# Optimization experiments

Measured on AMD Instinct MI355X. Metric: run time of the kernel, lower is better.

## Reference

```python
import jax, jax.numpy as jnp
import numpy as np
from functools import partial

N_NODES = 50000
N_EDGES = 800000
N_ENT = 100000
N_REL = 500
N_POS = 7            # sub_graph_hop_num + 2
DIM = 128            # node_emb_dim == rel_emb_dim == hidden_dim
HEADS = 8
HEAD_DIM = DIM // HEADS
HOPS = 3             # gnn_hop_num
ALPHA = 0.15
FFN_DIM = 4 * DIM
BATCH = 512
SLOPE = 0.2          # leaky relu negative slope


def _ln(x, g, b):
    mu = jnp.mean(x, axis=-1, keepdims=True)
    var = jnp.var(x, axis=-1, keepdims=True)
    return (x - mu) * jax.lax.rsqrt(var + 1e-5) * g + b


def _gdt_layer(h, src, dst, Wh, ah, at, g1, b1, w1, c1, w2, c2, g2, b2,
               rel_score=None):
    """Graph diffusion-transformer layer: edge-softmax attention + PPR hops."""
    N = h.shape[0]
    f = (h @ Wh).reshape(N, HEADS, HEAD_DIM)          # [N,H,Dh]
    s_src = jnp.sum(f * ah, axis=-1)                  # [N,H]
    s_dst = jnp.sum(f * at, axis=-1)                  # [N,H]
    e = s_src[src] + s_dst[dst]                       # [E,H]
    if rel_score is not None:
        e = e + rel_score
    e = jnp.where(e >= 0, e, SLOPE * e)               # leaky relu
    m = jax.ops.segment_max(e, dst, num_segments=N)   # [N,H]
    m = jnp.where(jnp.isfinite(m), m, 0.0)
    ex = jnp.exp(e - m[dst])
    den = jax.ops.segment_sum(ex, dst, num_segments=N)
    att = ex / (den[dst] + 1e-16)                     # [E,H] edge softmax

    feat0 = f
    def hop(feat, _):
        msg = feat[src] * att[:, :, None]             # [E,H,Dh]
        agg = jax.ops.segment_sum(msg, dst, num_segments=N)
        return ALPHA * feat0 + (1.0 - ALPHA) * agg, None
    feat, _ = jax.lax.scan(hop, feat0, None, length=HOPS)

    o = feat.reshape(N, DIM)
    o = _ln(o + h, g1, b1)                            # residual + LN
    ff = jax.nn.relu(o @ w1 + c1) @ w2 + c2           # FFN
    return _ln(o + ff, g2, b2)


def setup_inputs() -> dict:
    key = jax.random.key(0)
    ks = jax.random.split(key, 32)
    s = 0.05
    inp = {
        'ent_ids': jax.random.randint(ks[0], (N_NODES,), 0, N_ENT),
        'rel_ids': jax.random.randint(ks[1], (N_EDGES,), 0, N_REL),
        'arw_pos': jax.random.randint(ks[2], (N_NODES,), 0, N_POS),
        'src': jax.random.randint(ks[3], (N_EDGES,), 0, N_NODES),
        'dst': jax.random.randint(ks[4], (N_EDGES,), 0, N_NODES),
        'batch_node_ids': jax.random.randint(ks[5], (BATCH,), 0, N_NODES),
        'ent_tab': jax.random.normal(ks[6], (N_ENT, DIM)) * s,
        'rel_tab': jax.random.normal(ks[7], (N_REL, DIM)) * s,
        'pos_tab': jax.random.normal(ks[8], (N_POS, DIM)) * s,
        # layer 0 (RGDT: uses relation features)
        'l0_Wh': jax.random.normal(ks[9], (DIM, DIM)) * s,
        'l0_Wr': jax.random.normal(ks[10], (DIM, DIM)) * s,
        'l0_ah': jax.random.normal(ks[11], (HEADS, HEAD_DIM)) * s,
        'l0_at': jax.random.normal(ks[12], (HEADS, HEAD_DIM)) * s,
        'l0_ar': jax.random.normal(ks[13], (HEADS, HEAD_DIM)) * s,
        'l0_g1': jnp.ones((DIM,)), 'l0_b1': jnp.zeros((DIM,)),
        'l0_w1': jax.random.normal(ks[14], (DIM, FFN_DIM)) * s,
        'l0_c1': jnp.zeros((FFN_DIM,)),
        'l0_w2': jax.random.normal(ks[15], (FFN_DIM, DIM)) * s,
        'l0_c2': jnp.zeros((DIM,)),
        'l0_g2': jnp.ones((DIM,)), 'l0_b2': jnp.zeros((DIM,)),
        # layer 1 (GDT: no relation features)
        'l1_Wh': jax.random.normal(ks[16], (DIM, DIM)) * s,
        'l1_ah': jax.random.normal(ks[17], (HEADS, HEAD_DIM)) * s,
        'l1_at': jax.random.normal(ks[18], (HEADS, HEAD_DIM)) * s,
        'l1_g1': jnp.ones((DIM,)), 'l1_b1': jnp.zeros((DIM,)),
        'l1_w1': jax.random.normal(ks[19], (DIM, FFN_DIM)) * s,
        'l1_c1': jnp.zeros((FFN_DIM,)),
        'l1_w2': jax.random.normal(ks[20], (FFN_DIM, DIM)) * s,
        'l1_c2': jnp.zeros((DIM,)),
        'l1_g2': jnp.ones((DIM,)), 'l1_b2': jnp.zeros((DIM,)),
    }
    return inp


def reference(ent_ids, rel_ids, arw_pos, src, dst, batch_node_ids,
              ent_tab, rel_tab, pos_tab,
              l0_Wh, l0_Wr, l0_ah, l0_at, l0_ar, l0_g1, l0_b1,
              l0_w1, l0_c1, l0_w2, l0_c2, l0_g2, l0_b2,
              l1_Wh, l1_ah, l1_at, l1_g1, l1_b1,
              l1_w1, l1_c1, l1_w2, l1_c2, l1_g2, l1_b2):
    # embedding gathers + positional add
    h = ent_tab[ent_ids] + pos_tab[arw_pos]           # [N,D]
    rel = rel_tab[rel_ids]                            # [E,D]
    # relation contribution to layer-0 attention scores
    fr = (rel @ l0_Wr).reshape(-1, HEADS, HEAD_DIM)
    rel_score = jnp.sum(fr * l0_ar, axis=-1)          # [E,H]
    h = _gdt_layer(h, src, dst, l0_Wh, l0_ah, l0_at, l0_g1, l0_b1,
                   l0_w1, l0_c1, l0_w2, l0_c2, l0_g2, l0_b2,
                   rel_score=rel_score)
    h = _gdt_layer(h, src, dst, l1_Wh, l1_ah, l1_at, l1_g1, l1_b1,
                   l1_w1, l1_c1, l1_w2, l1_c2, l1_g2, l1_b2)
    return h[batch_node_ids]                          # [B,D] cls gather
```

## Files before the change

kernel.cpp:

```cpp
#include <hip/hip_runtime.h>
#include <hip/hip_bf16.h>

#define NNODES 50000
#define NEDGES 800000
#define NP 50048
#define DIM 128
#define HEADS 8
#define FFNDIM 512

typedef __bf16 bf16x8 __attribute__((ext_vector_type(8)));
typedef float f32x4 __attribute__((ext_vector_type(4)));
typedef unsigned int uint32;
typedef unsigned short ushort16;

__device__ __forceinline__ float b2f(uint32 u) {
  union { uint32 i; float f; } x; x.i = u << 16; return x.f;
}
__device__ __forceinline__ float b2fh(uint32 u) {
  union { uint32 i; float f; } x; x.i = u & 0xffff0000u; return x.f;
}
__device__ __forceinline__ ushort16 f2b(float f) {
  __bf16 h = (__bf16)f; return __builtin_bit_cast(ushort16, h);
}
__device__ __forceinline__ float h2f(unsigned short u) {
  return (float)__builtin_bit_cast(_Float16, u);
}
__device__ __forceinline__ unsigned short f2h(float f) {
  return __builtin_bit_cast(unsigned short, (_Float16)f);
}

__global__ void k_embed_hist(const int* __restrict__ ent_ids, const int* __restrict__ arw_pos,
                             const float* __restrict__ ent_tab, const float* __restrict__ pos_tab,
                             __bf16* __restrict__ hb, const int* __restrict__ dst,
                             int* __restrict__ deg) {
  int bid = blockIdx.x, tid = threadIdx.x;
  if (bid < 1563) {
    int t = bid * 256 + tid;
    if (t < NNODES * 8) {
      int n = t >> 3, c = t & 7;
      int e = ent_ids[n], a2 = arw_pos[n];
      #pragma unroll
      for (int i = 0; i < 4; ++i) {
        float4 a0 = ((const float4*)ent_tab)[e * 32 + c * 4 + i];
        float4 b0 = ((const float4*)pos_tab)[a2 * 32 + c * 4 + i];
        ushort4 o;
        o.x = f2b(a0.x + b0.x); o.y = f2b(a0.y + b0.y);
        o.z = f2b(a0.z + b0.z); o.w = f2b(a0.w + b0.w);
        ((ushort4*)hb)[n * 32 + c * 4 + i] = o;
      }
    }
  } else {
    int hbid = bid - 1563;
    int part = hbid & 7;
    int lo = part * 6250, hi2 = lo + 6250;
    for (int e = (hbid >> 3) * 256 + tid; e < NEDGES; e += 512 * 256) {
      int d = dst[e];
      if (d >= lo && d < hi2) atomicAdd(&deg[d], 1);
    }
  }
}

__global__ void k_prepA(const int* __restrict__ deg, int* __restrict__ csum,
                        const float* __restrict__ Wr, const float* __restrict__ ar,
                        const float* __restrict__ rel_tab, float* __restrict__ relsc,
                        const float* __restrict__ Wh0, const float* __restrict__ Wh1,
                        const float* __restrict__ w10, const float* __restrict__ w11,
                        const float* __restrict__ w20, const float* __restrict__ w21,
                        __bf16* __restrict__ T0, __bf16* __restrict__ T1,
                        __bf16* __restrict__ T2, __bf16* __restrict__ T3,
                        __bf16* __restrict__ T4, __bf16* __restrict__ T5) {
  int bid = blockIdx.x, tid = threadIdx.x;
  if (bid < 49) {
    __shared__ int ws[16];
    int lane = tid & 63, w = tid >> 6;
    int i = bid * 1024 + tid;
    int v = (i < NNODES) ? deg[i] : 0;
    #pragma unroll
    for (int o = 1; o < 64; o <<= 1) v += __shfl_xor(v, o);
    if (lane == 0) ws[w] = v;
    __syncthreads();
    if (tid == 0) {
      int s = 0;
      #pragma unroll
      for (int k = 0; k < 16; ++k) s += ws[k];
      csum[bid] = s;
    }
  } else if (bid <= 52) {
    __shared__ float vr[1024];
    int d = tid >> 3, hh = tid & 7;
    float s = 0.f;
    #pragma unroll
    for (int k = 0; k < 16; ++k) s += Wr[d * 128 + hh * 16 + k] * ar[hh * 16 + k];
    vr[tid] = s;
    __syncthreads();
    int t = (bid - 49) * 1024 + tid;
    if (t < 500 * 8) {
      int r = t >> 3, h2 = t & 7;
      float acc = 0.f;
      for (int dd = 0; dd < 128; ++dd) acc += rel_tab[r * 128 + dd] * vr[dd * 8 + h2];
      relsc[t] = acc;
    }
  } else {
    int wb = bid - 53;
    const float* W; __bf16* T; int lr2, lc2;
    int sub;
    if (wb < 16)        { W = Wh0; T = T0; lr2 = 7; lc2 = 7; sub = wb; }
    else if (wb < 32)   { W = Wh1; T = T1; lr2 = 7; lc2 = 7; sub = wb - 16; }
    else if (wb < 96)   { W = w10; T = T2; lr2 = 7; lc2 = 9; sub = wb - 32; }
    else if (wb < 160)  { W = w11; T = T3; lr2 = 7; lc2 = 9; sub = wb - 96; }
    else if (wb < 224)  { W = w20; T = T4; lr2 = 9; lc2 = 7; sub = wb - 160; }
    else                { W = w21; T = T5; lr2 = 9; lc2 = 7; sub = wb - 224; }
    int idx = sub * 1024 + tid;
    int r = idx & ((1 << lr2) - 1);
    int c = idx >> lr2;
    T[((long)c << lr2) + r] = (__bf16)W[((long)r << lc2) + c];
  }
}

__global__ void k_prepC(const int* __restrict__ deg, const int* __restrict__ csum,
                        int* __restrict__ rowptr, int* __restrict__ cursor) {
  __shared__ int wsum[16];
  __shared__ int s_coff, s_tot;
  int tid = threadIdx.x, lane = tid & 63, w = tid >> 6;
  if (tid < 64) {
    int v = (tid < 49) ? csum[tid] : 0;
    int x = v;
    #pragma unroll
    for (int o = 1; o < 64; o <<= 1) {
      int t = __shfl_up(x, o);
      if (tid >= o) x += t;
    }
    if (tid == (int)blockIdx.x) s_coff = x - v;
    if (tid == 48) s_tot = x;
  }
  int i = blockIdx.x * 1024 + tid;
  int v = (i < NNODES) ? deg[i] : 0;
  int x = v;
  #pragma unroll
  for (int o = 1; o < 64; o <<= 1) {
    int t = __shfl_up(x, o);
    if (lane >= o) x += t;
  }
  if (lane == 63) wsum[w] = x;
  __syncthreads();
  if (w == 0 && lane < 16) {
    int t = wsum[lane];
    #pragma unroll
    for (int o = 1; o < 16; o <<= 1) {
      int u = __shfl_up(t, o);
      if (lane >= o) t += u;
    }
    wsum[lane] = t;
  }
  __syncthreads();
  int add = s_coff + (w > 0 ? wsum[w - 1] : 0);
  if (i < NNODES) { rowptr[i] = add + x - v; cursor[i] = add + x - v; }
  if (blockIdx.x == 0 && tid == 0) rowptr[NNODES] = s_tot;
}

__global__ __launch_bounds__(256) void k_scatter(
    const int* __restrict__ dst, const int* __restrict__ src,
    const int* __restrict__ rel_ids, int* __restrict__ cursor,
    uint32* __restrict__ packed) {
  int part = blockIdx.x & 7;
  int lo = part * 6250, hi2 = lo + 6250;
  int tid = threadIdx.x;
  for (int e = (int)(blockIdx.x >> 3) * 256 + tid; e < NEDGES; e += 256 * 256) {
    int d = dst[e];
    if (d >= lo && d < hi2) {
      int p = atomicAdd(&cursor[d], 1);
      packed[p] = ((uint32)src[e] << 6) | ((uint32)rel_ids[e] << 22);
    }
  }
}

__global__ __launch_bounds__(256) void k_gemm0s(
    const __bf16* __restrict__ A, const __bf16* __restrict__ Bt,
    __bf16* __restrict__ fout, const float* __restrict__ ah, const float* __restrict__ at,
    float* __restrict__ ssrc, float* __restrict__ sdst) {
  __shared__ char sA[16384];
  __shared__ char sB[16384];
  const int tid = threadIdx.x;
  const int lane = tid & 63, wid = tid >> 6;
  const int wr = wid >> 1, wc = wid & 1;
  const int lr = lane & 15, hi = lane >> 4;
  const long row0 = (long)blockIdx.x * 128;
  f32x4 acc[4][4] = {};

  for (int kc = 0; kc < 2; ++kc) {
    __syncthreads();
    #pragma unroll
    for (int i = 0; i < 4; ++i) {
      int q = i * 256 + tid;
      int r = q >> 3, slot = q & 7;
      int sw = ((slot ^ (r & 7)) << 4);
      int4 av = *(const int4*)(A + (row0 + r) * 128 + kc * 64 + slot * 8);
      *(int4*)(sA + r * 128 + sw) = av;
      int4 bv = *(const int4*)(Bt + (long)r * 128 + kc * 64 + slot * 8);
      *(int4*)(sB + r * 128 + sw) = bv;
    }
    __syncthreads();
    #pragma unroll
    for (int ks = 0; ks < 2; ++ks) {
      bf16x8 af[4], bfr[4];
      #pragma unroll
      for (int m = 0; m < 4; ++m) {
        int r = wr * 64 + m * 16 + lr;
        int cb = ((ks * 4 + hi) ^ (r & 7)) << 4;
        af[m] = *(const bf16x8*)(sA + r * 128 + cb);
      }
      #pragma unroll
      for (int n = 0; n < 4; ++n) {
        int r = wc * 64 + n * 16 + lr;
        int cb = ((ks * 4 + hi) ^ (r & 7)) << 4;
        bfr[n] = *(const bf16x8*)(sB + r * 128 + cb);
      }
      #pragma unroll
      for (int m = 0; m < 4; ++m)
        #pragma unroll
        for (int n = 0; n < 4; ++n)
          acc[m][n] = __builtin_amdgcn_mfma_f32_16x16x32_bf16(af[m], bfr[n], acc[m][n], 0, 0, 0);
    }
  }

  float ahr[4], atr[4];
  #pragma unroll
  for (int n = 0; n < 4; ++n) {
    ahr[n] = ah[(wc * 4 + n) * 16 + lr];
    atr[n] = at[(wc * 4 + n) * 16 + lr];
  }
  #pragma unroll
  for (int m = 0; m < 4; ++m) {
    #pragma unroll
    for (int j = 0; j < 4; ++j) {
      long r = row0 + wr * 64 + m * 16 + hi * 4 + j;
      #pragma unroll
      for (int n = 0; n < 4; ++n) {
        long c = wc * 64 + n * 16 + lr;
        float v = acc[m][n][j];
        fout[r * 128 + c] = (__bf16)v;
        float ps = v * ahr[n], pt = v * atr[n];
        #pragma unroll
        for (int o = 1; o < 16; o <<= 1) { ps += __shfl_xor(ps, o); pt += __shfl_xor(pt, o); }
        if (lr == 0) {
          ssrc[r * 8 + wc * 4 + n] = ps;
          sdst[r * 8 + wc * 4 + n] = pt;
        }
      }
    }
  }
}

template<int KDIM, int NB>
__global__ __launch_bounds__(256) void k_gemm(
    const __bf16* __restrict__ A, const __bf16* __restrict__ Bt,
    const float* __restrict__ bias, __bf16* __restrict__ outb) {
  __shared__ char sA[16384];
  __shared__ char sB[16384];
  const int tid = threadIdx.x;
  const int lane = tid & 63, wid = tid >> 6;
  const int wr = wid >> 1, wc = wid & 1;
  const int lr = lane & 15, hi = lane >> 4;
  const long row0 = (long)blockIdx.x * 128;
  const long col0 = (long)blockIdx.y * 128;
  f32x4 acc[4][4] = {};

  for (int kc = 0; kc < KDIM / 64; ++kc) {
    __syncthreads();
    #pragma unroll
    for (int i = 0; i < 4; ++i) {
      int q = i * 256 + tid;
      int r = q >> 3, slot = q & 7;
      int sw = ((slot ^ (r & 7)) << 4);
      int4 av = *(const int4*)(A + (row0 + r) * KDIM + kc * 64 + slot * 8);
      *(int4*)(sA + r * 128 + sw) = av;
      int4 bv = *(const int4*)(Bt + (col0 + r) * KDIM + kc * 64 + slot * 8);
      *(int4*)(sB + r * 128 + sw) = bv;
    }
    __syncthreads();
    #pragma unroll
    for (int ks = 0; ks < 2; ++ks) {
      bf16x8 af[4], bfr[4];
      #pragma unroll
      for (int m = 0; m < 4; ++m) {
        int r = wr * 64 + m * 16 + lr;
        int cb = ((ks * 4 + hi) ^ (r & 7)) << 4;
        af[m] = *(const bf16x8*)(sA + r * 128 + cb);
      }
      #pragma unroll
      for (int n = 0; n < 4; ++n) {
        int r = wc * 64 + n * 16 + lr;
        int cb = ((ks * 4 + hi) ^ (r & 7)) << 4;
        bfr[n] = *(const bf16x8*)(sB + r * 128 + cb);
      }
      #pragma unroll
      for (int m = 0; m < 4; ++m)
        #pragma unroll
        for (int n = 0; n < 4; ++n)
          acc[m][n] = __builtin_amdgcn_mfma_f32_16x16x32_bf16(af[m], bfr[n], acc[m][n], 0, 0, 0);
    }
  }

  #pragma unroll
  for (int m = 0; m < 4; ++m) {
    #pragma unroll
    for (int j = 0; j < 4; ++j) {
      long r = row0 + wr * 64 + m * 16 + hi * 4 + j;
      #pragma unroll
      for (int n = 0; n < 4; ++n) {
        long c = col0 + wc * 64 + n * 16 + lr;
        outb[r * NB + c] = (__bf16)fmaxf(acc[m][n][j] + bias[c], 0.f);
      }
    }
  }
}

__global__ __launch_bounds__(256) void k_gemm2ln(
    const __bf16* __restrict__ A, const __bf16* __restrict__ Bt,
    const float* __restrict__ bias, const __bf16* __restrict__ resid,
    const float* __restrict__ g, const float* __restrict__ b,
    __bf16* __restrict__ outb, float* __restrict__ outf) {
  __shared__ char smem[65536];
  char* sA = smem;
  char* sB = smem + 16384;
  float* sV = (float*)smem;
  const int tid = threadIdx.x;
  const int lane = tid & 63, wid = tid >> 6;
  const int wr = wid >> 1, wc = wid & 1;
  const int lr = lane & 15, hi = lane >> 4;
  const long row0 = (long)blockIdx.x * 128;
  f32x4 acc[4][4] = {};

  for (int kc = 0; kc < 8; ++kc) {
    __syncthreads();
    #pragma unroll
    for (int i = 0; i < 4; ++i) {
      int q = i * 256 + tid;
      int r = q >> 3, slot = q & 7;
      int sw = ((slot ^ (r & 7)) << 4);
      int4 av = *(const int4*)(A + (row0 + r) * 512 + kc * 64 + slot * 8);
      *(int4*)(sA + r * 128 + sw) = av;
      int4 bv = *(const int4*)(Bt + (long)r * 512 + kc * 64 + slot * 8);
      *(int4*)(sB + r * 128 + sw) = bv;
    }
    __syncthreads();
    #pragma unroll
    for (int ks = 0; ks < 2; ++ks) {
      bf16x8 af[4], bfr[4];
      #pragma unroll
      for (int m = 0; m < 4; ++m) {
        int r = wr * 64 + m * 16 + lr;
        int cb = ((ks * 4 + hi) ^ (r & 7)) << 4;
        af[m] = *(const bf16x8*)(sA + r * 128 + cb);
      }
      #pragma unroll
      for (int n = 0; n < 4; ++n) {
        int r = wc * 64 + n * 16 + lr;
        int cb = ((ks * 4 + hi) ^ (r & 7)) << 4;
        bfr[n] = *(const bf16x8*)(sB + r * 128 + cb);
      }
      #pragma unroll
      for (int m = 0; m < 4; ++m)
        #pragma unroll
        for (int n = 0; n < 4; ++n)
          acc[m][n] = __builtin_amdgcn_mfma_f32_16x16x32_bf16(af[m], bfr[n], acc[m][n], 0, 0, 0);
    }
  }
  __syncthreads();

  float biasr[4];
  #pragma unroll
  for (int n = 0; n < 4; ++n) biasr[n] = bias[wc * 64 + n * 16 + lr];
  #pragma unroll
  for (int m = 0; m < 4; ++m) {
    #pragma unroll
    for (int j = 0; j < 4; ++j) {
      int rloc = wr * 64 + m * 16 + hi * 4 + j;
      long r = row0 + rloc;
      #pragma unroll
      for (int n = 0; n < 4; ++n) {
        int c = wc * 64 + n * 16 + lr;
        sV[rloc * 128 + c] = acc[m][n][j] + biasr[n] + (float)resid[r * 128 + c];
      }
    }
  }
  __syncthreads();

  float2 gg = ((const float2*)g)[lane];
  float2 bb = ((const float2*)b)[lane];
  for (int rr = 0; rr < 32; ++rr) {
    int rloc = wid * 32 + rr;
    long r = row0 + rloc;
    float2 v = ((float2*)sV)[rloc * 64 + lane];
    float x = v.x, y = v.y;
    float s = x + y;
    #pragma unroll
    for (int o = 1; o < 64; o <<= 1) s += __shfl_xor(s, o);
    float mean = s * (1.f / 128.f);
    float dx = x - mean, dy = y - mean;
    float q = dx * dx + dy * dy;
    #pragma unroll
    for (int o = 1; o < 64; o <<= 1) q += __shfl_xor(q, o);
    float rs = rsqrtf(q * (1.f / 128.f) + 1e-5f);
    float ox = dx * rs * gg.x + bb.x;
    float oy = dy * rs * gg.y + bb.y;
    if (outf) ((float2*)outf)[r * 64 + lane] = make_float2(ox, oy);
    ((uint32*)outb)[r * 64 + lane] = ((uint32)f2b(oy) << 16) | (uint32)f2b(ox);
  }
}

__global__ void k_softmax(const int* __restrict__ rowptr, const uint32* __restrict__ packed,
                          const float* __restrict__ ssrc, const float* __restrict__ sdst,
                          const float* __restrict__ relsc, unsigned short* __restrict__ att16) {
  int lane = threadIdx.x & 63, wid = threadIdx.x >> 6;
  int n = blockIdx.x * 4 + wid;
  if (n >= NNODES) return;
  int start = rowptr[n], end = rowptr[n + 1];
  if (start == end) return;
  int hh = lane & 7, jj = lane >> 3;
  float sd = sdst[n * 8 + hh];
  float m = -1e30f, den = 0.f;
  int deg = end - start;

  if (deg <= 64) {
    uint32 pk[8];
    float ev[8];
    int end1 = end - 1;
    #pragma unroll
    for (int t = 0; t < 8; ++t)
      pk[t] = packed[min(start + t * 8 + jj, end1)];
    #pragma unroll
    for (int t = 0; t < 8; ++t)
      ev[t] = ssrc[((pk[t] & 0x3fffffu) >> 3) | (uint32)hh];
    #pragma unroll
    for (int t = 0; t < 8; ++t) {
      int j = start + t * 8 + jj;
      float e = ev[t] + sd;
      if (relsc) e += relsc[((pk[t] >> 22) << 3) | (uint32)hh];
      e = (e >= 0.f) ? e : 0.2f * e;
      ev[t] = e;
      if (j < end) {
        float M = fmaxf(m, e);
        den = den * __expf(m - M) + __expf(e - M);
        m = M;
      }
    }
    #pragma unroll
    for (int o = 8; o < 64; o <<= 1) {
      float m2 = __shfl_xor(m, o), d2 = __shfl_xor(den, o);
      float M = fmaxf(m, m2);
      den = den * __expf(m - M) + d2 * __expf(m2 - M);
      m = M;
    }
    float inv = 1.f / (den + 1e-16f);
    #pragma unroll
    for (int t = 0; t < 8; ++t) {
      int j = start + t * 8 + jj;
      if (j < end) att16[j * 8 + hh] = f2h(__expf(ev[t] - m) * inv);
    }
  } else {
    for (int j0 = start; j0 < end; j0 += 8) {
      int j = j0 + jj;
      if (j < end) {
        uint32 p2 = packed[j];
        float e = ssrc[((p2 & 0x3fffffu) >> 3) | (uint32)hh] + sd;
        if (relsc) e += relsc[((p2 >> 22) << 3) | (uint32)hh];
        e = (e >= 0.f) ? e : 0.2f * e;
        att16[j * 8 + hh] = f2h(e);
        float M = fmaxf(m, e);
        den = den * __expf(m - M) + __expf(e - M);
        m = M;
      }
    }
    #pragma unroll
    for (int o = 8; o < 64; o <<= 1) {
      float m2 = __shfl_xor(m, o), d2 = __shfl_xor(den, o);
      float M = fmaxf(m, m2);
      den = den * __expf(m - M) + d2 * __expf(m2 - M);
      m = M;
    }
    float inv = 1.f / (den + 1e-16f);
    for (int j0 = start; j0 < end; j0 += 8) {
      int j = j0 + jj;
      if (j < end) att16[j * 8 + hh] = f2h(__expf(h2f(att16[j * 8 + hh]) - m) * inv);
    }
  }
}

template<int FINAL>
__global__ __launch_bounds__(256) void k_hop(
    const int* __restrict__ rowptr, const uint32* __restrict__ packed,
    const unsigned short* __restrict__ att16, const __bf16* __restrict__ fin,
    const __bf16* __restrict__ f0, __bf16* __restrict__ fout,
    const __bf16* __restrict__ resid, const float* __restrict__ g,
    const float* __restrict__ b) {
  int lane = threadIdx.x & 63, wid = threadIdx.x >> 6;
  int n = blockIdx.x * 4 + wid;
  if (n >= NNODES) return;
  uint32 z = ((const uint32*)f0)[n * 64 + lane];
  uint32 rz = 0u;
  if (FINAL) rz = ((const uint32*)resid)[n * 64 + lane];
  int start = rowptr[n], end = rowptr[n + 1];
  int hsel = lane >> 3;
  float ax = 0.f, ay = 0.f;
  const uint32* fin2 = (const uint32*)fin;
  int deg = end - start;
  int nfull = deg >> 4;
  int j0 = start;
  for (int bb2 = 0; bb2 < nfull; ++bb2, j0 += 16) {
    #pragma unroll
    for (int k = 0; k < 16; ++k) {
      float a = h2f(att16[(j0 + k) * 8 + hsel]);
      uint32 pk = packed[j0 + k];
      uint32 v = fin2[(pk & 0x3fffffu) | (uint32)lane];
      ax += a * b2f(v & 0xffffu);
      ay += a * b2fh(v);
    }
  }
  int nb = deg & 15;
  if (nb) {
    int end1 = end - 1;
    #pragma unroll
    for (int k = 0; k < 8; ++k) {
      int jc = min(j0 + k, end1);
      float a = h2f(att16[jc * 8 + hsel]);
      a = (k < nb) ? a : 0.f;
      uint32 pk = packed[jc];
      uint32 v = fin2[(pk & 0x3fffffu) | (uint32)lane];
      ax += a * b2f(v & 0xffffu);
      ay += a * b2fh(v);
    }
    if (nb > 8) {
      #pragma unroll
      for (int k = 8; k < 16; ++k) {
        int jc = min(j0 + k, end1);
        float a = h2f(att16[jc * 8 + hsel]);
        a = (k < nb) ? a : 0.f;
        uint32 pk = packed[jc];
        uint32 v = fin2[(pk & 0x3fffffu) | (uint32)lane];
        ax += a * b2f(v & 0xffffu);
        ay += a * b2fh(v);
      }
    }
  }
  float ox = 0.15f * b2f(z & 0xffffu) + 0.85f * ax;
  float oy = 0.15f * b2fh(z) + 0.85f * ay;
  if (!FINAL) {
    ((uint32*)fout)[n * 64 + lane] = ((uint32)f2b(oy) << 16) | (uint32)f2b(ox);
  } else {
    float x = ox + b2f(rz & 0xffffu);
    float y = oy + b2fh(rz);
    float s = x + y;
    #pragma unroll
    for (int o = 1; o < 64; o <<= 1) s += __shfl_xor(s, o);
    float mean = s * (1.f / 128.f);
    float dx = x - mean, dy = y - mean;
    float q = dx * dx + dy * dy;
    #pragma unroll
    for (int o = 1; o < 64; o <<= 1) q += __shfl_xor(q, o);
    float rs2 = rsqrtf(q * (1.f / 128.f) + 1e-5f);
    float2 gg = ((const float2*)g)[lane];
    float2 bb = ((const float2*)b)[lane];
    float o1 = dx * rs2 * gg.x + bb.x;
    float o2 = dy * rs2 * gg.y + bb.y;
    ((uint32*)fout)[n * 64 + lane] = ((uint32)f2b(o2) << 16) | (uint32)f2b(o1);
  }
}

__global__ void k_gather(const int* __restrict__ ids, const float* __restrict__ h,
                         float* __restrict__ out) {
  int t = blockIdx.x * 256 + threadIdx.x;
  if (t >= 512 * 32) return;
  int b = t >> 5, c = t & 31;
  ((float4*)out)[t] = ((const float4*)h)[(long)ids[b] * 32 + c];
}

struct LayerW {
  const float *Wh, *ah, *at, *g1, *b1, *w1, *c1, *w2, *c2, *g2, *b2;
};

extern "C" void kernel_launch(void* const* d_in, const int* in_sizes, int n_in,
                              void* d_out, int out_size, void* d_ws, size_t ws_size,
                              hipStream_t stream) {
  const int* ent_ids   = (const int*)d_in[0];
  const int* rel_ids   = (const int*)d_in[1];
  const int* arw_pos   = (const int*)d_in[2];
  const int* src       = (const int*)d_in[3];
  const int* dst       = (const int*)d_in[4];
  const int* batch_ids = (const int*)d_in[5];
  const float* ent_tab = (const float*)d_in[6];
  const float* rel_tab = (const float*)d_in[7];
  const float* pos_tab = (const float*)d_in[8];

  LayerW L0 = {(const float*)d_in[9],  (const float*)d_in[11], (const float*)d_in[12],
               (const float*)d_in[14], (const float*)d_in[15], (const float*)d_in[16],
               (const float*)d_in[17], (const float*)d_in[18], (const float*)d_in[19],
               (const float*)d_in[20], (const float*)d_in[21]};
  const float* l0_Wr = (const float*)d_in[10];
  const float* l0_ar = (const float*)d_in[13];
  LayerW L1 = {(const float*)d_in[22], (const float*)d_in[23], (const float*)d_in[24],
               (const float*)d_in[25], (const float*)d_in[26], (const float*)d_in[27],
               (const float*)d_in[28], (const float*)d_in[29], (const float*)d_in[30],
               (const float*)d_in[31], (const float*)d_in[32]};

  char* p = (char*)d_ws;
  auto alloc = [&](size_t bytes) { char* q = p; p += (bytes + 255) & ~(size_t)255; return q; };
  __bf16* hb = (__bf16*)alloc((size_t)NP * 128 * 2);
  __bf16* f  = (__bf16*)alloc((size_t)NP * 128 * 2);
  __bf16* fb = (__bf16*)alloc((size_t)NP * 128 * 2);
  __bf16* fa = (__bf16*)alloc((size_t)NP * 128 * 2);
  __bf16* ob = (__bf16*)alloc((size_t)NP * 128 * 2);
  char*   U  = alloc((size_t)NP * 512 * 2);
  unsigned short* att16 = (unsigned short*)U;
  __bf16* T   = (__bf16*)U;
  float*  y   = (float*)f;
  float* ssrc  = (float*)alloc((size_t)NP * 8 * 4);
  float* sdst  = (float*)alloc((size_t)NP * 8 * 4);
  float* relsc = (float*)alloc(500 * 8 * 4);
  __bf16* Wht0 = (__bf16*)alloc(128 * 128 * 2);
  __bf16* Wht1 = (__bf16*)alloc(128 * 128 * 2);
  __bf16* w1t0 = (__bf16*)alloc(512 * 128 * 2);
  __bf16* w1t1 = (__bf16*)alloc(512 * 128 * 2);
  __bf16* w2t0 = (__bf16*)alloc(128 * 512 * 2);
  __bf16* w2t1 = (__bf16*)alloc(128 * 512 * 2);
  int* deg    = (int*)alloc(NNODES * 4);
  int* rowptr = (int*)alloc((NNODES + 1) * 4);
  int* cursor = (int*)alloc(NNODES * 4);
  int* csum   = (int*)alloc(64 * 4);
  uint32* packed = (uint32*)alloc((size_t)NEDGES * 4);

  hipMemsetAsync(hb + (size_t)NNODES * 128, 0, (size_t)(NP - NNODES) * 128 * 2, stream);
  hipMemsetAsync(ob + (size_t)NNODES * 128, 0, (size_t)(NP - NNODES) * 128 * 2, stream);
  hipMemsetAsync(deg, 0, NNODES * sizeof(int), stream);

  k_embed_hist<<<1563 + 4096, 256, 0, stream>>>(ent_ids, arw_pos, ent_tab, pos_tab, hb, dst, deg);
  k_prepA<<<341, 1024, 0, stream>>>(deg, csum, l0_Wr, l0_ar, rel_tab, relsc,
                                    L0.Wh, L1.Wh, L0.w1, L1.w1, L0.w2, L1.w2,
                                    Wht0, Wht1, w1t0, w1t1, w2t0, w2t1);
  k_prepC<<<49, 1024, 0, stream>>>(deg, csum, rowptr, cursor);
  k_scatter<<<2048, 256, 0, stream>>>(dst, src, rel_ids, cursor, packed);

  const int NB4 = (NNODES + 3) / 4;
  for (int L = 0; L < 2; ++L) {
    const LayerW& W = L ? L1 : L0;
    const __bf16* Wht = L ? Wht1 : Wht0;
    const __bf16* w1t = L ? w1t1 : w1t0;
    const __bf16* w2t = L ? w2t1 : w2t0;
    const float* rsc  = L ? nullptr : relsc;

    k_gemm0s<<<391, 256, 0, stream>>>(hb, Wht, f, W.ah, W.at, ssrc, sdst);
    k_softmax<<<NB4, 256, 0, stream>>>(rowptr, packed, ssrc, sdst, rsc, att16);
    k_hop<0><<<NB4, 256, 0, stream>>>(rowptr, packed, att16, f, f, fa, nullptr, nullptr, nullptr);
    k_hop<0><<<NB4, 256, 0, stream>>>(rowptr, packed, att16, fa, f, fb, nullptr, nullptr, nullptr);
    k_hop<1><<<NB4, 256, 0, stream>>>(rowptr, packed, att16, fb, f, ob, hb, W.g1, W.b1);
    k_gemm<128, 512><<<dim3(391, 4), 256, 0, stream>>>(ob, w1t, W.c1, T);
    k_gemm2ln<<<391, 256, 0, stream>>>(T, w2t, W.c2, ob, W.g2, W.b2, hb,
                                       (L == 1) ? y : nullptr);
  }

  k_gather<<<64, 256, 0, stream>>>(batch_ids, y, (float*)d_out);
}
```

Measured before the change: 497.4 us.

## Fuse edge softmax with first diffusion hop and batch hop index loads

Result: faster. 477.1 us (-4.1%).

```diff
diff --git a/kernel.cpp b/kernel.cpp
--- a/kernel.cpp
+++ b/kernel.cpp
@@ -409,20 +409,24 @@
   }
 }
 
-__global__ void k_softmax(const int* __restrict__ rowptr, const uint32* __restrict__ packed,
-                          const float* __restrict__ ssrc, const float* __restrict__ sdst,
-                          const float* __restrict__ relsc, unsigned short* __restrict__ att16) {
+__global__ __launch_bounds__(256) void k_softhop(
+    const int* __restrict__ rowptr, const uint32* __restrict__ packed,
+    const float* __restrict__ ssrc, const float* __restrict__ sdst,
+    const float* __restrict__ relsc, unsigned short* __restrict__ att16,
+    const __bf16* __restrict__ f, __bf16* __restrict__ fout) {
   int lane = threadIdx.x & 63, wid = threadIdx.x >> 6;
   int n = blockIdx.x * 4 + wid;
   if (n >= NNODES) return;
+  uint32 z = ((const uint32*)f)[n * 64 + lane];
   int start = rowptr[n], end = rowptr[n + 1];
-  if (start == end) return;
+  int deg = end - start;
   int hh = lane & 7, jj = lane >> 3;
-  float sd = sdst[n * 8 + hh];
-  float m = -1e30f, den = 0.f;
-  int deg = end - start;
-
-  if (deg <= 64) {
+  int hsel = jj;
+  float ax = 0.f, ay = 0.f;
+  const uint32* fin2 = (const uint32*)f;
+
+  if (deg > 0 && deg <= 64) {
+    float sd = sdst[n * 8 + hh];
     uint32 pk[8];
     float ev[8];
     int end1 = end - 1;
@@ -432,14 +436,14 @@
     #pragma unroll
     for (int t = 0; t < 8; ++t)
       ev[t] = ssrc[((pk[t] & 0x3fffffu) >> 3) | (uint32)hh];
+    float m = -1e30f, den = 0.f;
     #pragma unroll
     for (int t = 0; t < 8; ++t) {
-      int j = start + t * 8 + jj;
       float e = ev[t] + sd;
       if (relsc) e += relsc[((pk[t] >> 22) << 3) | (uint32)hh];
       e = (e >= 0.f) ? e : 0.2f * e;
       ev[t] = e;
-      if (j < end) {
+      if (start + t * 8 + jj < end) {
         float M = fmaxf(m, e);
         den = den * __expf(m - M) + __expf(e - M);
         m = M;
@@ -455,10 +459,29 @@
     float inv = 1.f / (den + 1e-16f);
     #pragma unroll
     for (int t = 0; t < 8; ++t) {
+      ev[t] = __expf(ev[t] - m) * inv;
       int j = start + t * 8 + jj;
-      if (j < end) att16[j * 8 + hh] = f2h(__expf(ev[t] - m) * inv);
-    }
-  } else {
+      if (j < end) att16[j * 8 + hh] = f2h(ev[t]);
+    }
+    #pragma unroll
+    for (int tb = 0; tb < 4; ++tb) {
+      if (tb * 16 >= deg) break;
+      #pragma unroll
+      for (int i = 0; i < 16; ++i) {
+        int k = tb * 16 + i;
+        int t = tb * 2 + (i >> 3);
+        int sl = ((i & 7) << 3) + hsel;
+        float a = __shfl(ev[t], sl);
+        a = (k < deg) ? a : 0.f;
+        uint32 pkv = __shfl(pk[t], sl);
+        uint32 v = fin2[(pkv & 0x3fffffu) | (uint32)lane];
+        ax += a * b2f(v & 0xffffu);
+        ay += a * b2fh(v);
+      }
+    }
+  } else if (deg > 64) {
+    float sd = sdst[n * 8 + hh];
+    float m = -1e30f, den = 0.f;
     for (int j0 = start; j0 < end; j0 += 8) {
       int j = j0 + jj;
       if (j < end) {
@@ -484,7 +507,22 @@
       int j = j0 + jj;
       if (j < end) att16[j * 8 + hh] = f2h(__expf(h2f(att16[j * 8 + hh]) - m) * inv);
     }
-  }
+    for (int j = start; j < end; j += 16) {
+      #pragma unroll
+      for (int k = 0; k < 16; ++k) {
+        int jc = min(j + k, end - 1);
+        float a = h2f(att16[jc * 8 + hsel]);
+        a = (j + k < end) ? a : 0.f;
+        uint32 pkv = packed[jc];
+        uint32 v = fin2[(pkv & 0x3fffffu) | (uint32)lane];
+        ax += a * b2f(v & 0xffffu);
+        ay += a * b2fh(v);
+      }
+    }
+  }
+  float ox = 0.15f * b2f(z & 0xffffu) + 0.85f * ax;
+  float oy = 0.15f * b2fh(z) + 0.85f * ay;
+  ((uint32*)fout)[n * 64 + lane] = ((uint32)f2b(oy) << 16) | (uint32)f2b(ox);
 }
 
 template<int FINAL>
@@ -508,11 +546,16 @@
   int nfull = deg >> 4;
   int j0 = start;
   for (int bb2 = 0; bb2 < nfull; ++bb2, j0 += 16) {
+    uint32 pks[16];
+    unsigned short avs[16];
+    #pragma unroll
+    for (int k = 0; k < 16; ++k) pks[k] = packed[j0 + k];
+    #pragma unroll
+    for (int k = 0; k < 16; ++k) avs[k] = att16[(j0 + k) * 8 + hsel];
     #pragma unroll
     for (int k = 0; k < 16; ++k) {
-      float a = h2f(att16[(j0 + k) * 8 + hsel]);
-      uint32 pk = packed[j0 + k];
-      uint32 v = fin2[(pk & 0x3fffffu) | (uint32)lane];
+      uint32 v = fin2[(pks[k] & 0x3fffffu) | (uint32)lane];
+      float a = h2f(avs[k]);
       ax += a * b2f(v & 0xffffu);
       ay += a * b2fh(v);
     }
@@ -520,24 +563,38 @@
   int nb = deg & 15;
   if (nb) {
     int end1 = end - 1;
-    #pragma unroll
-    for (int k = 0; k < 8; ++k) {
-      int jc = min(j0 + k, end1);
-      float a = h2f(att16[jc * 8 + hsel]);
-      a = (k < nb) ? a : 0.f;
-      uint32 pk = packed[jc];
-      uint32 v = fin2[(pk & 0x3fffffu) | (uint32)lane];
-      ax += a * b2f(v & 0xffffu);
-      ay += a * b2fh(v);
+    {
+      uint32 pks[8];
+      unsigned short avs[8];
+      #pragma unroll
+      for (int k = 0; k < 8; ++k) {
+        int jc = min(j0 + k, end1);
+        pks[k] = packed[jc];
+        avs[k] = att16[jc * 8 + hsel];
+      }
+      #pragma unroll
+      for (int k = 0; k < 8; ++k) {
+        uint32 v = fin2[(pks[k] & 0x3fffffu) | (uint32)lane];
+        float a = h2f(avs[k]);
+        a = (k < nb) ? a : 0.f;
+        ax += a * b2f(v & 0xffffu);
+        ay += a * b2fh(v);
+      }
     }
     if (nb > 8) {
-      #pragma unroll
-      for (int k = 8; k < 16; ++k) {
-        int jc = min(j0 + k, end1);
-        float a = h2f(att16[jc * 8 + hsel]);
-        a = (k < nb) ? a : 0.f;
-        uint32 pk = packed[jc];
-        uint32 v = fin2[(pk & 0x3fffffu) | (uint32)lane];
+      uint32 pks[8];
+      unsigned short avs[8];
+      #pragma unroll
+      for (int k = 0; k < 8; ++k) {
+        int jc = min(j0 + 8 + k, end1);
+        pks[k] = packed[jc];
+        avs[k] = att16[jc * 8 + hsel];
+      }
+      #pragma unroll
+      for (int k = 0; k < 8; ++k) {
+        uint32 v = fin2[(pks[k] & 0x3fffffu) | (uint32)lane];
+        float a = h2f(avs[k]);
+        a = (8 + k < nb) ? a : 0.f;
         ax += a * b2f(v & 0xffffu);
         ay += a * b2fh(v);
       }
@@ -649,8 +706,7 @@
     const float* rsc  = L ? nullptr : relsc;
 
     k_gemm0s<<<391, 256, 0, stream>>>(hb, Wht, f, W.ah, W.at, ssrc, sdst);
-    k_softmax<<<NB4, 256, 0, stream>>>(rowptr, packed, ssrc, sdst, rsc, att16);
-    k_hop<0><<<NB4, 256, 0, stream>>>(rowptr, packed, att16, f, f, fa, nullptr, nullptr, nullptr);
+    k_softhop<<<NB4, 256, 0, stream>>>(rowptr, packed, ssrc, sdst, rsc, att16, f, fa);
     k_hop<0><<<NB4, 256, 0, stream>>>(rowptr, packed, att16, fa, f, fb, nullptr, nullptr, nullptr);
     k_hop<1><<<NB4, 256, 0, stream>>>(rowptr, packed, att16, fb, f, ob, hb, W.g1, W.b1);
     k_gemm<128, 512><<<dim3(391, 4), 256, 0, stream>>>(ob, w1t, W.c1, T);
```
